# Optimization experiments

Hardware: AMD Instinct MI355X
Metric: run time of the kernel (lower is better)

Reference implementation:

```python
import jax, jax.numpy as jnp
import numpy as np

BETA = 0.25
SCALE_NUM = 4  # len(latents_scale)


def setup_inputs() -> dict:
    key = jax.random.key(0)
    kz, ke = jax.random.split(key)
    z = jax.random.normal(kz, (8, 256, 32, 32), dtype=jnp.float32)
    emb_weight = jax.random.normal(ke, (16384, 256), dtype=jnp.float32) * 0.02
    return {"z": z, "emb_weight": emb_weight}


def reference(z, emb_weight):
    # z: [B, C, H, W] with C == vq_embed_dim and H == W (source reshapes with W twice)
    B, C, H, W = z.shape
    z_det = jax.lax.stop_gradient(z)

    # NOTE: in the source, `residual` is flattened ONCE before the scale loop and
    # never updated inside it, so every scale picks the same indices. We compute
    # the nearest-codebook assignment once (identical math, argmin of cdist is
    # invariant under sqrt, so squared distances suffice).
    residual = jnp.transpose(z_det, (0, 2, 3, 1)).reshape(-1, C)  # [N, D], N=B*H*W
    d2 = (jnp.sum(residual * residual, axis=1, keepdims=True)
          - 2.0 * residual @ emb_weight.T
          + jnp.sum(emb_weight * emb_weight, axis=1))  # [N, n_e]
    idx = jnp.argmin(d2, axis=1).reshape(B, W, W)  # [B, W, W]

    quantized = jnp.transpose(emb_weight[idx], (0, 3, 1, 2))  # [B, C, H, W]

    z_hat = jnp.zeros_like(z_det)
    loss = jnp.float32(0.0)
    for _ in range(SCALE_NUM):
        z_hat = z_hat + quantized
        loss = loss + BETA * jnp.mean((jax.lax.stop_gradient(z_hat) - z) ** 2) \
                    + jnp.mean((z_hat - z_det) ** 2)
    loss = loss / SCALE_NUM

    total_idx = jnp.concatenate([idx] * SCALE_NUM, axis=1)  # [B, SCALE_NUM*W, W]
    z_hat_out = z + jax.lax.stop_gradient(z_hat - z)  # straight-through
    return z_hat_out, loss, total_idx
```

## Files before the change

### kernel.cpp

```cpp
#include <hip/hip_runtime.h>

#define D      256
#define N_E    16384
#define NPTS   8192
#define ZOUT   2097152
#define MARGIN 2.0e-2f
#define STRIPS 4

typedef short bf16x8 __attribute__((ext_vector_type(8)));
typedef unsigned short us8 __attribute__((ext_vector_type(8)));
typedef float f32x16 __attribute__((ext_vector_type(16)));
typedef unsigned long long u64;

__device__ __forceinline__ unsigned short f2bf(float x) {
    unsigned int u = __float_as_uint(x);
    return (unsigned short)((u + 0x7FFFu + ((u >> 16) & 1u)) >> 16);
}
__device__ __forceinline__ void gl_lds16(const void* g, void* l) {
    __builtin_amdgcn_global_load_lds(
        (const __attribute__((address_space(1))) unsigned int*)g,
        (__attribute__((address_space(3))) unsigned int*)l, 16, 0, 0);
}

__global__ __launch_bounds__(256) void prep(
    const float* __restrict__ z, const float* __restrict__ emb,
    unsigned short* __restrict__ Zpk, float* __restrict__ Zf32,
    unsigned short* __restrict__ Epk, float* __restrict__ e2,
    float* __restrict__ loss) {
    const int t = threadIdx.x;
    if (blockIdx.x == 0 && t == 0) loss[0] = 0.f;
    if (blockIdx.x < 256) {
        const int n0 = blockIdx.x * 32;
        const int p = t & 31, ks8 = t >> 5;
        const int n = n0 + p;
        const int b = n >> 10, hw = n & 1023;
        const float* zb = z + (size_t)b * 262144 + hw;
        const int k0 = ks8 * 32;
        float v[32];
        #pragma unroll
        for (int kk = 0; kk < 32; ++kk)
            v[kk] = zb[(size_t)(k0 + kk) * 1024];
        #pragma unroll
        for (int i = 0; i < 8; ++i) {
            float4 f = {v[i * 4], v[i * 4 + 1], v[i * 4 + 2], v[i * 4 + 3]};
            *(float4*)(Zf32 + (size_t)n * D + k0 + i * 4) = f;
        }
        const int g = n >> 5;
        #pragma unroll
        for (int i = 0; i < 4; ++i) {
            us8 hv;
            #pragma unroll
            for (int c = 0; c < 8; ++c) hv[c] = f2bf(-2.0f * v[i * 8 + c]);
            const int kabs = k0 + i * 8;
            const int ks = kabs >> 4;
            const int l = (n & 31) + ((kabs >> 3) & 1) * 32;
            *(us8*)(Zpk + ((size_t)(g * 16 + ks) * 64 + l) * 8) = hv;
        }
    } else {
        const int j0 = (blockIdx.x - 256) * 32;
        const int jj = j0 + (t >> 3), q = t & 7;
        const float* row = emb + (size_t)jj * D + q * 32;
        float v[32];
        float s = 0.f;
        #pragma unroll
        for (int i = 0; i < 8; ++i) {
            const float4 x = *(const float4*)(row + i * 4);
            v[i * 4] = x.x; v[i * 4 + 1] = x.y; v[i * 4 + 2] = x.z; v[i * 4 + 3] = x.w;
            s += x.x * x.x + x.y * x.y + x.z * x.z + x.w * x.w;
        }
        const int g = jj >> 5;
        #pragma unroll
        for (int i = 0; i < 4; ++i) {
            us8 hv;
            #pragma unroll
            for (int c = 0; c < 8; ++c) hv[c] = f2bf(v[i * 8 + c]);
            const int kabs = q * 32 + i * 8;
            const int ks = kabs >> 4;
            const int l = (jj & 31) + ((kabs >> 3) & 1) * 32;
            *(us8*)(Epk + ((size_t)(g * 16 + ks) * 64 + l) * 8) = hv;
        }
        s += __shfl_xor(s, 1);
        s += __shfl_xor(s, 2);
        s += __shfl_xor(s, 4);
        if (q == 0) e2[jj] = s;
    }
}

__global__ __launch_bounds__(256, 2) void mfma_gemm(
    const unsigned short* __restrict__ Epk, const unsigned short* __restrict__ Zpk,
    const float* __restrict__ e2, float* __restrict__ tminv,
    u64* __restrict__ tmask) {
    __shared__ unsigned short Zbuf[64 * 512];

    const int tid = threadIdx.x, lane = tid & 63, wid = tid >> 6;
    const int c32 = lane & 31, l5 = lane >> 5;
    const int n0 = blockIdx.x * 128;
    const int cs0 = blockIdx.y * (STRIPS * 256);

    #pragma unroll
    for (int ks = 0; ks < 16; ++ks)
        gl_lds16(Zpk + ((size_t)((n0 >> 5) + wid) * 16 + ks) * 512 + lane * 8,
                 Zbuf + (wid * 16 + ks) * 512);
    __syncthreads();

    for (int s = 0; s < STRIPS; ++s) {
        const int cb = cs0 + s * 256 + wid * 64;
        const unsigned short* eb = Epk + ((size_t)(cb >> 5) * 16) * 512 + lane * 8;
        const unsigned short* zb = Zbuf + lane * 8;

        f32x16 acc[2][4];
        const f32x16 z16 = {0.f};
        #pragma unroll
        for (int i = 0; i < 2; ++i)
            #pragma unroll
            for (int j = 0; j < 4; ++j) acc[i][j] = z16;

        bf16x8 ec[2], pc[4];
        ec[0] = *(const bf16x8*)(eb);
        ec[1] = *(const bf16x8*)(eb + 16 * 512);
        #pragma unroll
        for (int j = 0; j < 4; ++j) pc[j] = *(const bf16x8*)(zb + (j * 16) * 512);

        #pragma unroll 4
        for (int ks = 0; ks < 16; ++ks) {
            bf16x8 en[2], pn[4];
            if (ks < 15) {
                en[0] = *(const bf16x8*)(eb + (ks + 1) * 512);
                en[1] = *(const bf16x8*)(eb + (16 + ks + 1) * 512);
                #pragma unroll
                for (int j = 0; j < 4; ++j)
                    pn[j] = *(const bf16x8*)(zb + (j * 16 + ks + 1) * 512);
            }
            #pragma unroll
            for (int i = 0; i < 2; ++i)
                #pragma unroll
                for (int j = 0; j < 4; ++j)
                    acc[i][j] = __builtin_amdgcn_mfma_f32_32x32x16_bf16(
                        ec[i], pc[j], acc[i][j], 0, 0, 0);
            if (ks < 15) {
                ec[0] = en[0]; ec[1] = en[1];
                #pragma unroll
                for (int j = 0; j < 4; ++j) pc[j] = pn[j];
            }
        }

        float e2r[2][16];
        #pragma unroll
        for (int i = 0; i < 2; ++i)
            #pragma unroll
            for (int r = 0; r < 16; ++r)
                e2r[i][r] = e2[cb + i * 32 + (r & 3) + 8 * (r >> 2) + 4 * l5];
        #pragma unroll
        for (int j = 0; j < 4; ++j) {
            float m = e2r[0][0] + acc[0][j][0];
            #pragma unroll
            for (int r = 1; r < 16; ++r) m = fminf(m, e2r[0][r] + acc[0][j][r]);
            #pragma unroll
            for (int r = 0; r < 16; ++r) m = fminf(m, e2r[1][r] + acc[1][j][r]);
            m = fminf(m, __shfl_xor(m, 32));
            const float th = m + MARGIN;
            unsigned mk[2];
            #pragma unroll
            for (int i = 0; i < 2; ++i) {
                unsigned mm = 0;
                #pragma unroll
                for (int r = 0; r < 16; ++r) {
                    const int row = (r & 3) + 8 * (r >> 2) + 4 * l5;
                    mm |= (e2r[i][r] + acc[i][j][r] <= th) ? (1u << row) : 0u;
                }
                mk[i] = mm | (unsigned)__shfl_xor((int)mm, 32);
            }
            if (l5 == 0) {
                const size_t pt = (size_t)(n0 + j * 32 + c32);
                tminv[pt * 256 + (cb >> 6)] = m;
                tmask[pt * 256 + (cb >> 6)] = ((u64)mk[1] << 32) | (u64)mk[0];
            }
        }
    }
}

__global__ __launch_bounds__(1024) void rescore_quant(
    const float* __restrict__ tminv, const u64* __restrict__ tmask,
    const float* __restrict__ Zf32, const float* __restrict__ emb,
    const float* __restrict__ e2, const float* __restrict__ z,
    float* __restrict__ out, float* __restrict__ out_idx,
    float* __restrict__ loss) {
    __shared__ int idx_s[32];
    __shared__ float wsum[16];
    const int tid = threadIdx.x, lane = tid & 63, wd = tid >> 6;
    const int n0 = blockIdx.x * 32;
    const int b = n0 >> 10, hw0 = n0 & 1023;

    #pragma unroll 1
    for (int p = 0; p < 2; ++p) {
        const int lp = wd * 2 + p;
        const int n = n0 + lp;
        const float4 zr = *(const float4*)(Zf32 + (size_t)n * D + lane * 4);
        const float4 tv = *(const float4*)(tminv + (size_t)n * 256 + lane * 4);

        float m1 = fminf(fminf(tv.x, tv.y), fminf(tv.z, tv.w));
        #pragma unroll
        for (int st = 1; st < 64; st <<= 1) m1 = fminf(m1, __shfl_xor(m1, st));
        const float thresh = m1 + MARGIN;

        u64 best = ~0ull;
        const float tva[4] = {tv.x, tv.y, tv.z, tv.w};
        #pragma unroll
        for (int k = 0; k < 4; ++k) {
            u64 gm = __ballot(tva[k] <= thresh);
            while (gm) {
                const int bit = (int)__builtin_ctzll(gm);
                gm &= gm - 1;
                const int g = bit * 4 + k;
                u64 cm = tmask[(size_t)n * 256 + g];
                while (cm) {
                    const int r = (int)__builtin_ctzll(cm);
                    cm &= cm - 1;
                    const int c = g * 64 + r;
                    const float4 ev = *(const float4*)(emb + (size_t)c * D + lane * 4);
                    float s = zr.x * ev.x + zr.y * ev.y + zr.z * ev.z + zr.w * ev.w;
                    #pragma unroll
                    for (int st = 1; st < 64; st <<= 1) s += __shfl_xor(s, st);
                    const float d = e2[c] - 2.0f * s;
                    unsigned int u = __float_as_uint(d);
                    u = (u & 0x80000000u) ? ~u : (u | 0x80000000u);
                    const u64 key = ((u64)u << 32) | (unsigned int)c;
                    if (key < best) best = key;
                }
            }
        }
        if (lane == 0)
            idx_s[lp] = (int)(unsigned int)(best & 0xFFFFFFFFull);
    }
    __syncthreads();

    if (tid < 32) {
        const float fv = (float)idx_s[tid];
        #pragma unroll
        for (int sc = 0; sc < 4; ++sc)
            out_idx[b * 4096 + sc * 1024 + hw0 + tid] = fv;
    }
    const int hw_l = tid & 31, cg = tid >> 5;
    const int j = idx_s[hw_l];
    const float* er = emb + (size_t)j * D + cg * 8;
    const float4 q0 = *(const float4*)er;
    const float4 q1 = *(const float4*)(er + 4);
    const float qv[8] = {q0.x, q0.y, q0.z, q0.w, q1.x, q1.y, q1.z, q1.w};
    float e = 0.f;
    #pragma unroll
    for (int cc = 0; cc < 8; ++cc) {
        const int c = cg * 8 + cc;
        const size_t zi = (size_t)b * 262144 + (size_t)c * 1024 + hw0 + hw_l;
        const float zv = z[zi];
        const float q = qv[cc];
        const float zh = ((q + q) + q) + q;
        out[zi] = zv + (zh - zv);
        e += 30.0f * q * q - 20.0f * q * zv + 4.0f * zv * zv;
    }
    #pragma unroll
    for (int off = 32; off > 0; off >>= 1) e += __shfl_down(e, off);
    if (lane == 0) wsum[wd] = e;
    __syncthreads();
    if (tid == 0) {
        float s = 0.f;
        #pragma unroll
        for (int i = 0; i < 16; ++i) s += wsum[i];
        atomicAdd(loss, s * (0.3125f / 2097152.0f));
    }
}

extern "C" void kernel_launch(void* const* d_in, const int* in_sizes, int n_in,
                              void* d_out, int out_size, void* d_ws, size_t ws_size,
                              hipStream_t stream) {
    const float* z = (const float*)d_in[0];
    const float* emb = (const float*)d_in[1];
    float* out = (float*)d_out;

    unsigned short* Zpk = (unsigned short*)d_ws;
    unsigned short* Epk = Zpk + (size_t)NPTS * D;
    float* Zf32 = (float*)(Epk + (size_t)N_E * D);
    float* e2 = Zf32 + (size_t)NPTS * D;
    float* tminv = e2 + N_E;
    u64* tmask = (u64*)(tminv + (size_t)NPTS * 256);

    float* loss = out + ZOUT;
    float* out_idx = out + ZOUT + 1;

    prep<<<768, 256, 0, stream>>>(z, emb, Zpk, Zf32, Epk, e2, loss);
    mfma_gemm<<<dim3(NPTS / 128, N_E / (256 * STRIPS)), 256, 0, stream>>>(
        Epk, Zpk, e2, tminv, tmask);
    rescore_quant<<<256, 1024, 0, stream>>>(tminv, tmask, Zf32, emb, e2, z,
                                            out, out_idx, loss);
}
```

Measured before the change: 161.9 us.

## Fold codebook norms into the MFMA via an extra bf16 K-slice

Each codebook group gets a 17th packed K-slice that holds the squared norm split into bf16 hi/lo parts. After the main K loop, one extra MFMA per accumulator against a constant vector of ones adds e2 directly into the accumulators, so the 32 per-lane e2 global loads and the adds in the epilogue go away. The E-operand prefetch also becomes two-deep, which adds registers. The hi+lo bf16 split of e2 carries a small rounding error, which the selection margin should tolerate.

```diff
diff --git a/kernel.cpp b/kernel.cpp
--- a/kernel.cpp
+++ b/kernel.cpp
@@ -6,6 +6,7 @@
 #define ZOUT   2097152
 #define MARGIN 2.0e-2f
 #define STRIPS 4
+#define ECH    17
 
 typedef short bf16x8 __attribute__((ext_vector_type(8)));
 typedef unsigned short us8 __attribute__((ext_vector_type(8)));
@@ -15,6 +16,9 @@
 __device__ __forceinline__ unsigned short f2bf(float x) {
     unsigned int u = __float_as_uint(x);
     return (unsigned short)((u + 0x7FFFu + ((u >> 16) & 1u)) >> 16);
+}
+__device__ __forceinline__ float bf2f(unsigned short h) {
+    return __uint_as_float((unsigned int)h << 16);
 }
 __device__ __forceinline__ void gl_lds16(const void* g, void* l) {
     __builtin_amdgcn_global_load_lds(
@@ -27,6 +31,7 @@
     unsigned short* __restrict__ Zpk, float* __restrict__ Zf32,
     unsigned short* __restrict__ Epk, float* __restrict__ e2,
     float* __restrict__ loss) {
+    __shared__ float sh[32];
     const int t = threadIdx.x;
     if (blockIdx.x == 0 && t == 0) loss[0] = 0.f;
     if (blockIdx.x < 256) {
@@ -57,7 +62,8 @@
             *(us8*)(Zpk + ((size_t)(g * 16 + ks) * 64 + l) * 8) = hv;
         }
     } else {
-        const int j0 = (blockIdx.x - 256) * 32;
+        const int bi = blockIdx.x - 256;
+        const int j0 = bi * 32;
         const int jj = j0 + (t >> 3), q = t & 7;
         const float* row = emb + (size_t)jj * D + q * 32;
         float v[32];
@@ -68,7 +74,6 @@
             v[i * 4] = x.x; v[i * 4 + 1] = x.y; v[i * 4 + 2] = x.z; v[i * 4 + 3] = x.w;
             s += x.x * x.x + x.y * x.y + x.z * x.z + x.w * x.w;
         }
-        const int g = jj >> 5;
         #pragma unroll
         for (int i = 0; i < 4; ++i) {
             us8 hv;
@@ -77,25 +82,43 @@
             const int kabs = q * 32 + i * 8;
             const int ks = kabs >> 4;
             const int l = (jj & 31) + ((kabs >> 3) & 1) * 32;
-            *(us8*)(Epk + ((size_t)(g * 16 + ks) * 64 + l) * 8) = hv;
+            *(us8*)(Epk + ((size_t)(bi * ECH + ks) * 64 + l) * 8) = hv;
         }
         s += __shfl_xor(s, 1);
         s += __shfl_xor(s, 2);
         s += __shfl_xor(s, 4);
-        if (q == 0) e2[jj] = s;
+        if (q == 0) { e2[jj] = s; sh[t >> 3] = s; }
+        __syncthreads();
+        if (t < 64) {
+            us8 hv;
+            #pragma unroll
+            for (int c = 0; c < 8; ++c) hv[c] = 0;
+            if (t < 32) {
+                const float vv = sh[t];
+                const unsigned short hi = f2bf(vv);
+                hv[0] = hi;
+                hv[1] = f2bf(vv - bf2f(hi));
+            }
+            *(us8*)(Epk + ((size_t)bi * ECH + 16) * 512 + t * 8) = hv;
+        }
     }
 }
 
 __global__ __launch_bounds__(256, 2) void mfma_gemm(
     const unsigned short* __restrict__ Epk, const unsigned short* __restrict__ Zpk,
-    const float* __restrict__ e2, float* __restrict__ tminv,
-    u64* __restrict__ tmask) {
+    float* __restrict__ tminv, u64* __restrict__ tmask) {
     __shared__ unsigned short Zbuf[64 * 512];
 
     const int tid = threadIdx.x, lane = tid & 63, wid = tid >> 6;
     const int c32 = lane & 31, l5 = lane >> 5;
     const int n0 = blockIdx.x * 128;
     const int cs0 = blockIdx.y * (STRIPS * 256);
+
+    us8 puu;
+    #pragma unroll
+    for (int c = 0; c < 8; ++c) puu[c] = 0;
+    if (l5 == 0) { puu[0] = 0x3F80; puu[1] = 0x3F80; }
+    const bf16x8 pu = (bf16x8)puu;
 
     #pragma unroll
     for (int ks = 0; ks < 16; ++ks)
@@ -105,7 +128,8 @@
 
     for (int s = 0; s < STRIPS; ++s) {
         const int cb = cs0 + s * 256 + wid * 64;
-        const unsigned short* eb = Epk + ((size_t)(cb >> 5) * 16) * 512 + lane * 8;
+        const unsigned short* eb =
+            Epk + ((size_t)(cb >> 5) * ECH) * 512 + lane * 8;
         const unsigned short* zb = Zbuf + lane * 8;
 
         f32x16 acc[2][4];
@@ -115,48 +139,58 @@
             #pragma unroll
             for (int j = 0; j < 4; ++j) acc[i][j] = z16;
 
-        bf16x8 ec[2], pc[4];
-        ec[0] = *(const bf16x8*)(eb);
-        ec[1] = *(const bf16x8*)(eb + 16 * 512);
+        bf16x8 eq0a = *(const bf16x8*)(eb);
+        bf16x8 eq0b = *(const bf16x8*)(eb + ECH * 512);
+        bf16x8 eq1a = *(const bf16x8*)(eb + 512);
+        bf16x8 eq1b = *(const bf16x8*)(eb + ECH * 512 + 512);
+        bf16x8 pc[4], pn[4];
         #pragma unroll
         for (int j = 0; j < 4; ++j) pc[j] = *(const bf16x8*)(zb + (j * 16) * 512);
 
         #pragma unroll 4
         for (int ks = 0; ks < 16; ++ks) {
-            bf16x8 en[2], pn[4];
+            bf16x8 ef0, ef1;
+            if ((ks & 1) == 0) { ef0 = eq0a; ef1 = eq0b; }
+            else               { ef0 = eq1a; ef1 = eq1b; }
             if (ks < 15) {
-                en[0] = *(const bf16x8*)(eb + (ks + 1) * 512);
-                en[1] = *(const bf16x8*)(eb + (16 + ks + 1) * 512);
+                const unsigned short* ep = eb + (ks + 2) * 512;
+                if ((ks & 1) == 0) {
+                    eq0a = *(const bf16x8*)ep;
+                    eq0b = *(const bf16x8*)(ep + ECH * 512);
+                } else {
+                    eq1a = *(const bf16x8*)ep;
+                    eq1b = *(const bf16x8*)(ep + ECH * 512);
+                }
                 #pragma unroll
                 for (int j = 0; j < 4; ++j)
                     pn[j] = *(const bf16x8*)(zb + (j * 16 + ks + 1) * 512);
             }
-            #pragma unroll
-            for (int i = 0; i < 2; ++i)
-                #pragma unroll
-                for (int j = 0; j < 4; ++j)
-                    acc[i][j] = __builtin_amdgcn_mfma_f32_32x32x16_bf16(
-                        ec[i], pc[j], acc[i][j], 0, 0, 0);
+            acc[0][0] = __builtin_amdgcn_mfma_f32_32x32x16_bf16(ef0, pc[0], acc[0][0], 0, 0, 0);
+            acc[0][1] = __builtin_amdgcn_mfma_f32_32x32x16_bf16(ef0, pc[1], acc[0][1], 0, 0, 0);
+            acc[0][2] = __builtin_amdgcn_mfma_f32_32x32x16_bf16(ef0, pc[2], acc[0][2], 0, 0, 0);
+            acc[0][3] = __builtin_amdgcn_mfma_f32_32x32x16_bf16(ef0, pc[3], acc[0][3], 0, 0, 0);
+            acc[1][0] = __builtin_amdgcn_mfma_f32_32x32x16_bf16(ef1, pc[0], acc[1][0], 0, 0, 0);
+            acc[1][1] = __builtin_amdgcn_mfma_f32_32x32x16_bf16(ef1, pc[1], acc[1][1], 0, 0, 0);
+            acc[1][2] = __builtin_amdgcn_mfma_f32_32x32x16_bf16(ef1, pc[2], acc[1][2], 0, 0, 0);
+            acc[1][3] = __builtin_amdgcn_mfma_f32_32x32x16_bf16(ef1, pc[3], acc[1][3], 0, 0, 0);
             if (ks < 15) {
-                ec[0] = en[0]; ec[1] = en[1];
                 #pragma unroll
                 for (int j = 0; j < 4; ++j) pc[j] = pn[j];
             }
         }
-
-        float e2r[2][16];
-        #pragma unroll
-        for (int i = 0; i < 2; ++i)
-            #pragma unroll
-            for (int r = 0; r < 16; ++r)
-                e2r[i][r] = e2[cb + i * 32 + (r & 3) + 8 * (r >> 2) + 4 * l5];
         #pragma unroll
         for (int j = 0; j < 4; ++j) {
-            float m = e2r[0][0] + acc[0][j][0];
-            #pragma unroll
-            for (int r = 1; r < 16; ++r) m = fminf(m, e2r[0][r] + acc[0][j][r]);
-            #pragma unroll
-            for (int r = 0; r < 16; ++r) m = fminf(m, e2r[1][r] + acc[1][j][r]);
+            acc[0][j] = __builtin_amdgcn_mfma_f32_32x32x16_bf16(eq0a, pu, acc[0][j], 0, 0, 0);
+            acc[1][j] = __builtin_amdgcn_mfma_f32_32x32x16_bf16(eq0b, pu, acc[1][j], 0, 0, 0);
+        }
+
+        #pragma unroll
+        for (int j = 0; j < 4; ++j) {
+            float m = acc[0][j][0];
+            #pragma unroll
+            for (int r = 1; r < 16; ++r) m = fminf(m, acc[0][j][r]);
+            #pragma unroll
+            for (int r = 0; r < 16; ++r) m = fminf(m, acc[1][j][r]);
             m = fminf(m, __shfl_xor(m, 32));
             const float th = m + MARGIN;
             unsigned mk[2];
@@ -166,7 +200,7 @@
                 #pragma unroll
                 for (int r = 0; r < 16; ++r) {
                     const int row = (r & 3) + 8 * (r >> 2) + 4 * l5;
-                    mm |= (e2r[i][r] + acc[i][j][r] <= th) ? (1u << row) : 0u;
+                    mm |= (acc[i][j][r] <= th) ? (1u << row) : 0u;
                 }
                 mk[i] = mm | (unsigned)__shfl_xor((int)mm, 32);
             }
@@ -278,7 +312,7 @@
 
     unsigned short* Zpk = (unsigned short*)d_ws;
     unsigned short* Epk = Zpk + (size_t)NPTS * D;
-    float* Zf32 = (float*)(Epk + (size_t)N_E * D);
+    float* Zf32 = (float*)(Epk + (size_t)(N_E / 32) * ECH * 512);
     float* e2 = Zf32 + (size_t)NPTS * D;
     float* tminv = e2 + N_E;
     u64* tmask = (u64*)(tminv + (size_t)NPTS * 256);
@@ -288,7 +322,7 @@
 
     prep<<<768, 256, 0, stream>>>(z, emb, Zpk, Zf32, Epk, e2, loss);
     mfma_gemm<<<dim3(NPTS / 128, N_E / (256 * STRIPS)), 256, 0, stream>>>(
-        Epk, Zpk, e2, tminv, tmask);
+        Epk, Zpk, tminv, tmask);
     rescore_quant<<<256, 1024, 0, stream>>>(tminv, tmask, Zf32, emb, e2, z,
                                             out, out_idx, loss);
 }
```

New measurement: 161.6 us. No clear change (-0.2%).
